# Optimization experiments

Measured on AMD Instinct MI355X. Metric: run time of the kernel, lower is better.

## Reference

```python
import jax, jax.numpy as jnp
import numpy as np

# SelectiveAttention (keras) reference.
# - A single shared InputDense (D -> key_dim) projects query, key, value.
# - ComponentBuilder yields (filter_input=Q, context_input=banded K^T, _input=V):
#   scores = (Q K^T / sqrt(key_dim)) masked to the band |i-j| <= band_size
#   (the layer's Softmax sublayer is built but never invoked in call()).
# - attended = scores @ V, then OutputDense (key_dim -> D). Dropout inactive at inference.

def setup_inputs() -> dict:
    key = jax.random.key(0)
    ks = jax.random.split(key, 5)
    B, S, D, Dk = 4, 4096, 512, 64
    query = jax.random.normal(ks[0], (B, S, D), dtype=jnp.float32)
    value = jax.random.normal(ks[1], (B, S, D), dtype=jnp.float32)
    Wi = jax.random.normal(ks[2], (D, Dk), dtype=jnp.float32) * (1.0 / np.sqrt(D))
    bi = jnp.zeros((Dk,), dtype=jnp.float32)
    Wo = jax.random.normal(ks[3], (Dk, D), dtype=jnp.float32) * (1.0 / np.sqrt(Dk))
    bo = jnp.zeros((D,), dtype=jnp.float32)
    return {"query": query, "value": value, "Wi": Wi, "bi": bi,
            "Wo": Wo, "bo": bo, "band_size": 128}


def reference(query, value, Wi, bi, Wo, bo, band_size):
    Dk = Wi.shape[1]
    scale = 1.0 / jnp.sqrt(jnp.asarray(Dk, dtype=query.dtype))
    # shared input projection (same dense for q, k, v; key defaults to value)
    q = query @ Wi + bi            # [B,S,Dk]
    kv = value @ Wi + bi           # [B,S,Dk]  (k == v here)
    scores = jnp.einsum('bqd,bkd->bqk', q, kv) * scale  # [B,S,S]
    S = q.shape[1]
    idx = jnp.arange(S)
    band = (jnp.abs(idx[:, None] - idx[None, :]) <= band_size)  # [S,S] bool
    scores = jnp.where(band[None], scores, 0.0)
    attended = jnp.einsum('bqk,bkd->bqd', scores, kv)    # [B,S,Dk]
    return attended @ Wo + bo                            # [B,S,D]
```

## Files before the change

### kernel.cpp

```cpp
#include <hip/hip_runtime.h>
#include <math.h>


typedef __bf16 bf16;
using bf16x4  = __attribute__((ext_vector_type(4))) __bf16;
using bf16x8  = __attribute__((ext_vector_type(8))) __bf16;
using floatx4 = __attribute__((ext_vector_type(4))) float;

#define MFMA(a, b, c) __builtin_amdgcn_mfma_f32_16x16x32_bf16(a, b, c, 0, 0, 0)

__global__ __launch_bounds__(256) void prep_weights(
    const float* __restrict__ Wi, const float* __restrict__ Wo,
    bf16* __restrict__ WiT, bf16* __restrict__ WoT)
{
    __shared__ float T[64][65];
    const int blk = blockIdx.x, tid = threadIdx.x;
    if (blk < 8) {
        const int k0 = blk * 64;
        #pragma unroll
        for (int i = 0; i < 4; i++) {
            int idx4 = tid * 4 + i;
            int r = idx4 >> 4, c4 = (idx4 & 15) * 4;
            float4 f = *(const float4*)(Wi + (size_t)(k0 + r) * 64 + c4);
            T[r][c4 + 0] = f.x; T[r][c4 + 1] = f.y;
            T[r][c4 + 2] = f.z; T[r][c4 + 3] = f.w;
        }
        __syncthreads();
        #pragma unroll
        for (int i = 0; i < 2; i++) {
            int seg = tid * 2 + i;
            int n = seg >> 3, k8 = (seg & 7) * 8;
            bf16x8 v;
            #pragma unroll
            for (int j = 0; j < 8; j++) v[j] = (bf16)T[k8 + j][n];
            *(bf16x8*)(WiT + (size_t)n * 512 + k0 + k8) = v;
        }
    } else {
        const int n0 = (blk - 8) * 64;
        #pragma unroll
        for (int i = 0; i < 4; i++) {
            int idx4 = tid * 4 + i;
            int r = idx4 >> 4, c4 = (idx4 & 15) * 4;
            float4 f = *(const float4*)(Wo + (size_t)r * 512 + n0 + c4);
            T[r][c4 + 0] = f.x; T[r][c4 + 1] = f.y;
            T[r][c4 + 2] = f.z; T[r][c4 + 3] = f.w;
        }
        __syncthreads();
        #pragma unroll
        for (int i = 0; i < 2; i++) {
            int seg = tid * 2 + i;
            int n = seg >> 3, k8 = (seg & 7) * 8;
            bf16x8 v;
            #pragma unroll
            for (int j = 0; j < 8; j++) v[j] = (bf16)T[k8 + j][n];
            *(bf16x8*)(WoT + (size_t)(n0 + n) * 64 + k8) = v;
        }
    }
}

__global__ __launch_bounds__(256, 4) void proj_in_kernel(
    const float* __restrict__ v, const bf16* __restrict__ WiT,
    const float* __restrict__ bi, bf16* __restrict__ kvp,
    bf16* __restrict__ kvT, int K, int S)
{
    __shared__ float P[4][16][68];
    const int tid = threadIdx.x;
    const int wave = tid >> 6, lane = tid & 63;
    const int lr = lane & 15, lq = lane >> 4;
    const int row0 = blockIdx.x * 16;
    const float* xrow = v + (size_t)(row0 + lr) * K + wave * 128;
    const bf16* wrow = WiT + wave * 128;

    floatx4 acc[4] = {};
    #pragma unroll
    for (int ks = 0; ks < 4; ks++) {
        const int k0 = ks * 32 + lq * 8;
        float4 a0 = *(const float4*)(xrow + k0);
        float4 a1 = *(const float4*)(xrow + k0 + 4);
        bf16x8 af;
        af[0] = (bf16)a0.x; af[1] = (bf16)a0.y; af[2] = (bf16)a0.z; af[3] = (bf16)a0.w;
        af[4] = (bf16)a1.x; af[5] = (bf16)a1.y; af[6] = (bf16)a1.z; af[7] = (bf16)a1.w;
        #pragma unroll
        for (int t = 0; t < 4; t++) {
            bf16x8 bfv = *(const bf16x8*)(wrow + (size_t)(t * 16 + lr) * K + k0);
            acc[t] = MFMA(af, bfv, acc[t]);
        }
    }
    #pragma unroll
    for (int t = 0; t < 4; t++)
        #pragma unroll
        for (int r = 0; r < 4; r++)
            P[wave][lq * 4 + r][t * 16 + lr] = acc[t][r];
    __syncthreads();

    {
        const int row = tid >> 4, c4 = (tid & 15) * 4;
        float4 s0 = *(const float4*)&P[0][row][c4];
        float4 s1 = *(const float4*)&P[1][row][c4];
        float4 s2 = *(const float4*)&P[2][row][c4];
        float4 s3 = *(const float4*)&P[3][row][c4];
        float4 bb = *(const float4*)(bi + c4);
        bf16x4 o;
        o[0] = (bf16)(s0.x + s1.x + s2.x + s3.x + bb.x);
        o[1] = (bf16)(s0.y + s1.y + s2.y + s3.y + bb.y);
        o[2] = (bf16)(s0.z + s1.z + s2.z + s3.z + bb.z);
        o[3] = (bf16)(s0.w + s1.w + s2.w + s3.w + bb.w);
        *(bf16x4*)(kvp + (size_t)(row0 + row) * 64 + c4) = o;
    }
    {
        const int d = tid >> 2, s4 = (tid & 3) * 4;
        const int b = row0 >> 12, s0r = row0 & (S - 1);
        const float bb = bi[d];
        bf16x4 o;
        #pragma unroll
        for (int i = 0; i < 4; i++) {
            float s = P[0][s4 + i][d] + P[1][s4 + i][d]
                    + P[2][s4 + i][d] + P[3][s4 + i][d] + bb;
            o[i] = (bf16)s;
        }
        *(bf16x4*)(kvT + ((size_t)b * 64 + d) * S + s0r + s4) = o;
    }
}

__global__ __launch_bounds__(256, 4) void band_attn_out_kernel(
    const float* __restrict__ query, const bf16* __restrict__ WiT,
    const float* __restrict__ bi, const bf16* __restrict__ kvp,
    const bf16* __restrict__ kvT, const int* __restrict__ band_ptr,
    const bf16* __restrict__ WoT, const float* __restrict__ bo,
    float* __restrict__ out, int K, int S, float scale)
{
    __shared__ float P[4][16][68];
    __shared__ bf16 Ss[16][344];
    __shared__ bf16 St[16][88];
    const int tid = threadIdx.x;
    const int wave = tid >> 6, lane = tid & 63;
    const int lr = lane & 15, lq = lane >> 4;
    const int gs = blockIdx.x;
    const int b = gs >> 8;
    const int q0 = (gs & 255) * 16;
    const int band = band_ptr[0];

    {
        const float* xrow = query + ((size_t)b * S + q0 + lr) * K + wave * 128;
        const bf16* wrow = WiT + wave * 128;
        floatx4 qa[4] = {};
        #pragma unroll
        for (int ks = 0; ks < 4; ks++) {
            const int k0 = ks * 32 + lq * 8;
            float4 a0 = *(const float4*)(xrow + k0);
            float4 a1 = *(const float4*)(xrow + k0 + 4);
            bf16x8 af;
            af[0] = (bf16)a0.x; af[1] = (bf16)a0.y; af[2] = (bf16)a0.z; af[3] = (bf16)a0.w;
            af[4] = (bf16)a1.x; af[5] = (bf16)a1.y; af[6] = (bf16)a1.z; af[7] = (bf16)a1.w;
            #pragma unroll
            for (int t = 0; t < 4; t++) {
                bf16x8 bfv = *(const bf16x8*)(wrow + (size_t)(t * 16 + lr) * K + k0);
                qa[t] = MFMA(af, bfv, qa[t]);
            }
        }
        #pragma unroll
        for (int t = 0; t < 4; t++)
            #pragma unroll
            for (int r = 0; r < 4; r++)
                P[wave][lq * 4 + r][t * 16 + lr] = qa[t][r];
    }
    __syncthreads();
    {
        const int row = tid >> 4, c4 = (tid & 15) * 4;
        float4 s0 = *(const float4*)&P[0][row][c4];
        float4 s1 = *(const float4*)&P[1][row][c4];
        float4 s2 = *(const float4*)&P[2][row][c4];
        float4 s3 = *(const float4*)&P[3][row][c4];
        float4 bb = *(const float4*)(bi + c4);
        bf16x4 o;
        o[0] = (bf16)((s0.x + s1.x + s2.x + s3.x + bb.x) * scale);
        o[1] = (bf16)((s0.y + s1.y + s2.y + s3.y + bb.y) * scale);
        o[2] = (bf16)((s0.z + s1.z + s2.z + s3.z + bb.z) * scale);
        o[3] = (bf16)((s0.w + s1.w + s2.w + s3.w + bb.w) * scale);
        *(bf16x4*)(&St[row][c4]) = o;
    }
    __syncthreads();
    bf16x8 qf0 = *(const bf16x8*)(&St[lr][lq * 8]);
    bf16x8 qf1 = *(const bf16x8*)(&St[lr][32 + lq * 8]);

    const int base = ((q0 - band) >> 6) * 64;
    #pragma unroll
    for (int i = 0; i < 3; i++) {
        const int h = wave + i * 4;
        if (h < 10) {
            const int kj0 = base + h * 32;
            floatx4 sc[2] = {};
            #pragma unroll
            for (int t2 = 0; t2 < 2; t2++) {
                int kr = kj0 + t2 * 16 + lr;
                int krc = min(max(kr, 0), S - 1);
                const bf16* kp = kvp + ((size_t)b * S + krc) * 64;
                bf16x8 b0 = *(const bf16x8*)(kp + lq * 8);
                bf16x8 b1 = *(const bf16x8*)(kp + 32 + lq * 8);
                sc[t2] = MFMA(qf0, b0, sc[t2]);
                sc[t2] = MFMA(qf1, b1, sc[t2]);
            }
            #pragma unroll
            for (int t2 = 0; t2 < 2; t2++) {
                int kj = kj0 + t2 * 16 + lr;
                bool kv_ok = (kj >= 0) && (kj < S);
                #pragma unroll
                for (int r = 0; r < 4; r++) {
                    int qi = q0 + lq * 4 + r;
                    int dlt = qi - kj; dlt = dlt < 0 ? -dlt : dlt;
                    float vv = (kv_ok && dlt <= band) ? sc[t2][r] : 0.f;
                    Ss[lq * 4 + r][h * 32 + t2 * 16 + lr] = (bf16)vv;
                }
            }
        }
    }
    __syncthreads();

    {
        floatx4 acc = {};
        const bf16* vrow = kvT + ((size_t)b * 64 + wave * 16 + lr) * S;
        #pragma unroll
        for (int h = 0; h < 10; h++) {
            bf16x8 sa = *(const bf16x8*)(&Ss[lr][h * 32 + lq * 8]);
            int kb = base + h * 32 + lq * 8;
            int kbc = min(max(kb, 0), S - 8);
            bf16x8 vb = *(const bf16x8*)(vrow + kbc);
            acc = MFMA(sa, vb, acc);
        }
        #pragma unroll
        for (int r = 0; r < 4; r++)
            St[lq * 4 + r][wave * 16 + lr] = (bf16)acc[r];
    }
    __syncthreads();

    bf16x8 af0 = *(const bf16x8*)(&St[lr][lq * 8]);
    bf16x8 af1 = *(const bf16x8*)(&St[lr][32 + lq * 8]);
    float* orow = out + ((size_t)b * S + q0) * 512;
    #pragma unroll
    for (int i = 0; i < 8; i++) {
        const int tp = wave * 8 + i;
        const bf16* wp = WoT + (size_t)(tp * 16 + lr) * 64;
        bf16x8 w0 = *(const bf16x8*)(wp + lq * 8);
        bf16x8 w1 = *(const bf16x8*)(wp + 32 + lq * 8);
        floatx4 o = {};
        o = MFMA(w0, af0, o);
        o = MFMA(w1, af1, o);
        float4 bb = *(const float4*)(bo + tp * 16 + lq * 4);
        float4 ov;
        ov.x = o[0] + bb.x; ov.y = o[1] + bb.y;
        ov.z = o[2] + bb.z; ov.w = o[3] + bb.w;
        *(float4*)(orow + (size_t)lr * 512 + tp * 16 + lq * 4) = ov;
    }
}

extern "C" void kernel_launch(void* const* d_in, const int* in_sizes, int n_in,
                              void* d_out, int out_size, void* d_ws, size_t ws_size,
                              hipStream_t stream) {
    const float* query = (const float*)d_in[0];
    const float* value = (const float*)d_in[1];
    const float* Wi    = (const float*)d_in[2];
    const float* bi    = (const float*)d_in[3];
    const float* Wo    = (const float*)d_in[4];
    const float* bo    = (const float*)d_in[5];
    const int*   band  = (const int*)d_in[6];
    float* out = (float*)d_out;

    const int Dk = in_sizes[3];
    const int D  = in_sizes[5];
    const int S  = 4096;
    const int BS = in_sizes[0] / D;
    const int B  = BS / S;
    const float scale = 1.0f / sqrtf((float)Dk);

    bf16* WiT = (bf16*)d_ws;
    bf16* WoT = WiT + 32768;
    bf16* kvp = WoT + 32768;
    bf16* kvT = kvp + (size_t)BS * 64;

    prep_weights<<<16, 256, 0, stream>>>(Wi, Wo, WiT, WoT);

    proj_in_kernel<<<dim3(BS / 16), 256, 0, stream>>>(
        value, WiT, bi, kvp, kvT, D, S);

    band_attn_out_kernel<<<dim3(BS / 16), 256, 0, stream>>>(
        query, WiT, bi, kvp, kvT, band, WoT, bo, out, D, S, scale);
}
```

Baseline: 148.8 us.

## Run banded attention block as a single wave, drop barriers and partial sums

The attention/output kernel now runs one 64-thread wave per 16-query tile instead of four waves. That one wave does the full Q projection over K=512, all score tiles, all four V column tiles and all 32 output tiles. This removes the cross-wave LDS partial-sum reduction and every __syncthreads. It also adds a fast path that skips per-element band masking for 32-key tiles lying fully inside the band. In exchange each block has four times less parallelism and a longer serial chain per wave, so latency hiding now rests on running more blocks at once.

```diff
diff --git a/kernel.cpp b/kernel.cpp
--- a/kernel.cpp
+++ b/kernel.cpp
@@ -122,18 +122,16 @@
     }
 }
 
-__global__ __launch_bounds__(256, 4) void band_attn_out_kernel(
+__global__ __launch_bounds__(64, 2) void band_attn_out_kernel(
     const float* __restrict__ query, const bf16* __restrict__ WiT,
     const float* __restrict__ bi, const bf16* __restrict__ kvp,
     const bf16* __restrict__ kvT, const int* __restrict__ band_ptr,
     const bf16* __restrict__ WoT, const float* __restrict__ bo,
     float* __restrict__ out, int K, int S, float scale)
 {
-    __shared__ float P[4][16][68];
-    __shared__ bf16 Ss[16][344];
-    __shared__ bf16 St[16][88];
-    const int tid = threadIdx.x;
-    const int wave = tid >> 6, lane = tid & 63;
+    __shared__ bf16 Qs[16][80];
+    __shared__ bf16 Ss[16][336];
+    const int lane = threadIdx.x;
     const int lr = lane & 15, lq = lane >> 4;
     const int gs = blockIdx.x;
     const int b = gs >> 8;
@@ -141,11 +139,10 @@
     const int band = band_ptr[0];
 
     {
-        const float* xrow = query + ((size_t)b * S + q0 + lr) * K + wave * 128;
-        const bf16* wrow = WiT + wave * 128;
+        const float* xrow = query + ((size_t)b * S + q0 + lr) * K;
         floatx4 qa[4] = {};
         #pragma unroll
-        for (int ks = 0; ks < 4; ks++) {
+        for (int ks = 0; ks < 16; ks++) {
             const int k0 = ks * 32 + lq * 8;
             float4 a0 = *(const float4*)(xrow + k0);
             float4 a1 = *(const float4*)(xrow + k0 + 4);
@@ -154,52 +151,46 @@
             af[4] = (bf16)a1.x; af[5] = (bf16)a1.y; af[6] = (bf16)a1.z; af[7] = (bf16)a1.w;
             #pragma unroll
             for (int t = 0; t < 4; t++) {
-                bf16x8 bfv = *(const bf16x8*)(wrow + (size_t)(t * 16 + lr) * K + k0);
+                bf16x8 bfv = *(const bf16x8*)(WiT + (size_t)(t * 16 + lr) * K + k0);
                 qa[t] = MFMA(af, bfv, qa[t]);
             }
         }
         #pragma unroll
-        for (int t = 0; t < 4; t++)
+        for (int t = 0; t < 4; t++) {
+            float bb = bi[t * 16 + lr];
             #pragma unroll
             for (int r = 0; r < 4; r++)
-                P[wave][lq * 4 + r][t * 16 + lr] = qa[t][r];
-    }
-    __syncthreads();
-    {
-        const int row = tid >> 4, c4 = (tid & 15) * 4;
-        float4 s0 = *(const float4*)&P[0][row][c4];
-        float4 s1 = *(const float4*)&P[1][row][c4];
-        float4 s2 = *(const float4*)&P[2][row][c4];
-        float4 s3 = *(const float4*)&P[3][row][c4];
-        float4 bb = *(const float4*)(bi + c4);
-        bf16x4 o;
-        o[0] = (bf16)((s0.x + s1.x + s2.x + s3.x + bb.x) * scale);
-        o[1] = (bf16)((s0.y + s1.y + s2.y + s3.y + bb.y) * scale);
-        o[2] = (bf16)((s0.z + s1.z + s2.z + s3.z + bb.z) * scale);
-        o[3] = (bf16)((s0.w + s1.w + s2.w + s3.w + bb.w) * scale);
-        *(bf16x4*)(&St[row][c4]) = o;
-    }
-    __syncthreads();
-    bf16x8 qf0 = *(const bf16x8*)(&St[lr][lq * 8]);
-    bf16x8 qf1 = *(const bf16x8*)(&St[lr][32 + lq * 8]);
+                Qs[lq * 4 + r][t * 16 + lr] = (bf16)((qa[t][r] + bb) * scale);
+        }
+    }
+    bf16x8 qf0 = *(const bf16x8*)(&Qs[lr][lq * 8]);
+    bf16x8 qf1 = *(const bf16x8*)(&Qs[lr][32 + lq * 8]);
 
     const int base = ((q0 - band) >> 6) * 64;
     #pragma unroll
-    for (int i = 0; i < 3; i++) {
-        const int h = wave + i * 4;
-        if (h < 10) {
-            const int kj0 = base + h * 32;
-            floatx4 sc[2] = {};
-            #pragma unroll
-            for (int t2 = 0; t2 < 2; t2++) {
-                int kr = kj0 + t2 * 16 + lr;
-                int krc = min(max(kr, 0), S - 1);
-                const bf16* kp = kvp + ((size_t)b * S + krc) * 64;
-                bf16x8 b0 = *(const bf16x8*)(kp + lq * 8);
-                bf16x8 b1 = *(const bf16x8*)(kp + 32 + lq * 8);
-                sc[t2] = MFMA(qf0, b0, sc[t2]);
-                sc[t2] = MFMA(qf1, b1, sc[t2]);
-            }
+    for (int h = 0; h < 10; h++) {
+        const int kj0 = base + h * 32;
+        floatx4 sc[2] = {};
+        #pragma unroll
+        for (int t2 = 0; t2 < 2; t2++) {
+            int kr = kj0 + t2 * 16 + lr;
+            int krc = min(max(kr, 0), S - 1);
+            const bf16* kp = kvp + ((size_t)b * S + krc) * 64;
+            bf16x8 b0 = *(const bf16x8*)(kp + lq * 8);
+            bf16x8 b1 = *(const bf16x8*)(kp + 32 + lq * 8);
+            sc[t2] = MFMA(qf0, b0, sc[t2]);
+            sc[t2] = MFMA(qf1, b1, sc[t2]);
+        }
+        const int lo = kj0, hi = kj0 + 31;
+        const bool full = (lo >= 0) && (hi < S) &&
+                          (lo >= q0 + 15 - band) && (hi <= q0 + band);
+        if (full) {
+            #pragma unroll
+            for (int t2 = 0; t2 < 2; t2++)
+                #pragma unroll
+                for (int r = 0; r < 4; r++)
+                    Ss[lq * 4 + r][h * 32 + t2 * 16 + lr] = (bf16)sc[t2][r];
+        } else {
             #pragma unroll
             for (int t2 = 0; t2 < 2; t2++) {
                 int kj = kj0 + t2 * 16 + lr;
@@ -214,31 +205,30 @@
             }
         }
     }
-    __syncthreads();
-
-    {
-        floatx4 acc = {};
-        const bf16* vrow = kvT + ((size_t)b * 64 + wave * 16 + lr) * S;
-        #pragma unroll
-        for (int h = 0; h < 10; h++) {
-            bf16x8 sa = *(const bf16x8*)(&Ss[lr][h * 32 + lq * 8]);
-            int kb = base + h * 32 + lq * 8;
-            int kbc = min(max(kb, 0), S - 8);
-            bf16x8 vb = *(const bf16x8*)(vrow + kbc);
-            acc = MFMA(sa, vb, acc);
-        }
+
+    floatx4 acc[4] = {};
+    #pragma unroll
+    for (int h = 0; h < 10; h++) {
+        bf16x8 sa = *(const bf16x8*)(&Ss[lr][h * 32 + lq * 8]);
+        int kb = base + h * 32 + lq * 8;
+        int kbc = min(max(kb, 0), S - 8);
+        #pragma unroll
+        for (int t = 0; t < 4; t++) {
+            bf16x8 vb = *(const bf16x8*)(kvT + ((size_t)b * 64 + t * 16 + lr) * S + kbc);
+            acc[t] = MFMA(sa, vb, acc[t]);
+        }
+    }
+    #pragma unroll
+    for (int t = 0; t < 4; t++)
         #pragma unroll
         for (int r = 0; r < 4; r++)
-            St[lq * 4 + r][wave * 16 + lr] = (bf16)acc[r];
-    }
-    __syncthreads();
-
-    bf16x8 af0 = *(const bf16x8*)(&St[lr][lq * 8]);
-    bf16x8 af1 = *(const bf16x8*)(&St[lr][32 + lq * 8]);
+            Qs[lq * 4 + r][t * 16 + lr] = (bf16)acc[t][r];
+    bf16x8 af0 = *(const bf16x8*)(&Qs[lr][lq * 8]);
+    bf16x8 af1 = *(const bf16x8*)(&Qs[lr][32 + lq * 8]);
+
     float* orow = out + ((size_t)b * S + q0) * 512;
     #pragma unroll
-    for (int i = 0; i < 8; i++) {
-        const int tp = wave * 8 + i;
+    for (int tp = 0; tp < 32; tp++) {
         const bf16* wp = WoT + (size_t)(tp * 16 + lr) * 64;
         bf16x8 w0 = *(const bf16x8*)(wp + lq * 8);
         bf16x8 w1 = *(const bf16x8*)(wp + 32 + lq * 8);
@@ -282,6 +272,6 @@
     proj_in_kernel<<<dim3(BS / 16), 256, 0, stream>>>(
         value, WiT, bi, kvp, kvT, D, S);
 
-    band_attn_out_kernel<<<dim3(BS / 16), 256, 0, stream>>>(
+    band_attn_out_kernel<<<dim3(BS / 16), 64, 0, stream>>>(
         query, WiT, bi, kvp, kvT, band, WoT, bo, out, D, S, scale);
 }
```

Result: faster. 145.1 us (-2.5%).
